# Kernel optimization log

Measured on AMD Instinct MI355X. Metric: run time of the kernel, lower is better.

The kernel has to match this reference:

```python
import jax, jax.numpy as jnp
import numpy as np

B, C_IN, H, W = 32, 64, 64, 64
D, O, S_SP, K = 256, 512, 4, 3


def setup_inputs() -> dict:
    key = jax.random.key(0)
    k1, k2, k3, k4, k5 = jax.random.split(key, 5)
    x = jax.random.normal(k1, (B, C_IN, H, W), dtype=jnp.float32)
    dictionary = jax.random.normal(k2, (D, C_IN, K, K), dtype=jnp.float32)
    lookup_coefficients = jax.random.normal(k3, (O, S_SP), dtype=jnp.float32)
    bias = jax.random.normal(k4, (O,), dtype=jnp.float32)
    lookup_indices = jax.random.randint(k5, (O, S_SP), 0, D)
    return {
        "x": x,
        "dictionary": dictionary,
        "lookup_coefficients": lookup_coefficients,
        "bias": bias,
        "lookup_indices": lookup_indices,
    }


def reference(x, dictionary, lookup_coefficients, bias, lookup_indices):
    # Dictionary conv: S has shape [B, D, H, W] (stride 1, padding 1, 3x3 kernel)
    S = jax.lax.conv_general_dilated(
        x, dictionary,
        window_strides=(1, 1),
        padding=((1, 1), (1, 1)),
        dimension_numbers=("NCHW", "OIHW", "NCHW"),
    )
    # Build dense [O, D] combine matrix via scatter-add (duplicate indices
    # accumulate, matching the original += loop), then one GEMM.
    rows = jnp.arange(O)[:, None]  # [O, 1] broadcast against [O, sparsity]
    Wc = jnp.zeros((O, D), dtype=S.dtype).at[rows, lookup_indices].add(lookup_coefficients)
    out = jnp.einsum("bdhw,od->bohw", S, Wc)
    return out + bias[None, :, None, None]
```

## Files before the change

### kernel.cpp

```cpp
#include <hip/hip_runtime.h>
#include <stdint.h>

#define NB 32
#define NC 64
#define NH 64
#define NW 64
#define NO 512
#define ND 256
#define HP 66

typedef __bf16 bf16x8 __attribute__((ext_vector_type(8)));
typedef short  s16x8  __attribute__((ext_vector_type(8)));
typedef float  f32x4  __attribute__((ext_vector_type(4)));
typedef uint32_t u32x2 __attribute__((ext_vector_type(2)));

__device__ __forceinline__ uint16_t f2bf(float f) {
  uint32_t u = __builtin_bit_cast(uint32_t, f);
  u += 0x7fffu + ((u >> 16) & 1u);
  return (uint16_t)(u >> 16);
}
__device__ __forceinline__ uint32_t pk2(float a, float b) {
  return (uint32_t)f2bf(a) | ((uint32_t)f2bf(b) << 16);
}
__device__ __forceinline__ float ubf_lo(uint32_t u) {
  return __builtin_bit_cast(float, u << 16);
}
__device__ __forceinline__ float ubf_hi(uint32_t u) {
  return __builtin_bit_cast(float, u & 0xffff0000u);
}

__device__ __forceinline__ void gld16(const uint16_t* g, uint16_t* l) {
  __builtin_amdgcn_global_load_lds(
      (const __attribute__((address_space(1))) void*)(g),
      (__attribute__((address_space(3))) void*)(l), 16, 0, 0);
}

__global__ void k_prep(const float* __restrict__ dict,
                       const float* __restrict__ x,
                       uint16_t*    __restrict__ Wd,
                       uint16_t*    __restrict__ xh) {
  const int bid = blockIdx.x;
  const int t = threadIdx.x;
  if (bid < ND) {
    const int d = bid;
#pragma unroll
    for (int j = 0; j < 3; ++j) {
      const int id = t + j * 256;
      if (id < 576) {
        const int c = id & 63, p = id >> 6;
        const int sl = ((p * ND + d) * 8 + ((c >> 3) ^ (d & 7))) * 8 + (c & 7);
        Wd[sl] = f2bf(dict[d * 576 + c * 9 + p]);
      }
    }
    return;
  }
  const int bh = bid - ND;
  const int b = bh / HP, hp = bh % HP;
  uint16_t* row = xh + (size_t)(b * HP + hp) * 4096;
  int4* r4 = reinterpret_cast<int4*>(row);
  if (hp == 0 || hp == HP - 1) {
    r4[t]       = int4{0, 0, 0, 0};
    r4[t + 256] = int4{0, 0, 0, 0};
    return;
  }
  __shared__ float tile[64][65];
  const int h = hp - 1;
  const int w = t & 63;
#pragma unroll
  for (int c = (t >> 6); c < 64; c += 4)
    tile[c][w] = x[((size_t)(b * NC + c) * NH + h) * NW + w];
  __syncthreads();
#pragma unroll
  for (int i = 0; i < 2; ++i) {
    const int s = t + i * 256;
    const int w2 = s >> 3, cb = s & 7;
    uint32_t dd[4];
#pragma unroll
    for (int j = 0; j < 4; ++j)
      dd[j] = pk2(tile[cb * 8 + 2 * j][w2], tile[cb * 8 + 2 * j + 1][w2]);
    r4[w2 * 8 + (cb ^ (w2 & 7))] =
        int4{(int)dd[0], (int)dd[1], (int)dd[2], (int)dd[3]};
  }
}

__global__ __launch_bounds__(512, 2) void k_conv(
    const uint16_t* __restrict__ xh,
    const uint16_t* __restrict__ Wd,
    const float*    __restrict__ coef,
    const int*      __restrict__ idx,
    const float*    __restrict__ bias,
    float*          __restrict__ out) {
  __shared__ __align__(16) uint16_t smem[74496];
  uint16_t* xs  = smem;
  uint16_t* asw = smem + 25344;
  uint8_t*  Sb  = (uint8_t*)smem;

  const int t = threadIdx.x;
  const int lane = t & 63;
  const int wid  = t >> 6;
  const int flat = blockIdx.x;
  const int s    = (flat & 7) * 64 + (flat >> 3);
  const int b    = s >> 4;
  const int hq   = s & 15;
  const int h0p  = hq * 4;

  if (t < 96) {
    const int r = t >> 4, sl = (t >> 3) & 1, j = t & 7;
    reinterpret_cast<int4*>(xs)[r * 528 + sl * 520 + j] = int4{0, 0, 0, 0};
  }
  {
#pragma unroll
    for (int j = 0; j < 6; ++j) {
      const int ch = wid * 6 + j;
      const int r = ch >> 3, k = ch & 7;
      gld16(xh + (size_t)(b * HP + h0p + r) * 4096 + k * 512 + lane * 8,
            xs + r * 4224 + 64 + k * 512);
    }
  }
  auto stage_a = [&](int g) {
#pragma unroll
    for (int j = 0; j < 12; ++j) {
      const int ch = wid * 12 + j;
      const int tap = ch >> 5, k = ch & 31;
      gld16(Wd + (size_t)(tap * 3 + g) * 16384 + k * 512 + lane * 8,
            asw + tap * 16384 + k * 512);
    }
  };
  stage_a(0);

  const int wd  = wid & 3;
  const int wn  = wid >> 2;
  const int l15 = lane & 15;
  const int lg  = lane >> 4;

  f32x4 acc[8][4];
#pragma unroll
  for (int pb = 0; pb < 8; ++pb)
#pragma unroll
    for (int db = 0; db < 4; ++db)
      acc[pb][db] = (f32x4){0.f, 0.f, 0.f, 0.f};

  __syncthreads();

#pragma unroll
  for (int g = 0; g < 3; ++g) {
    const int dw = g - 1;
#pragma unroll
    for (int q = 0; q < 2; ++q) {
      const int cbB = (q * 4 + lg) ^ ((l15 + dw) & 7);
      const uint16_t* xb = xs + (l15 + dw + 1) * 64 + cbB * 8;
      bf16x8 braw[4][4];
#pragma unroll
      for (int rr = 0; rr < 4; ++rr)
#pragma unroll
        for (int nw = 0; nw < 4; ++nw)
          braw[rr][nw] = __builtin_bit_cast(bf16x8,
              *reinterpret_cast<const s16x8*>(
                  xb + (wn * 2 + rr) * 4224 + nw * 1024));
      const int cbA = (q * 4 + lg) ^ (l15 & 7);
      const uint16_t* ab = asw + (wd * 64 + l15) * 64 + cbA * 8;
#pragma unroll
      for (int dh = 0; dh < 3; ++dh) {
        bf16x8 af[4];
#pragma unroll
        for (int db = 0; db < 4; ++db)
          af[db] = __builtin_bit_cast(bf16x8,
              *reinterpret_cast<const s16x8*>(
                  ab + dh * 16384 + db * 1024));
#pragma unroll
        for (int pb = 0; pb < 8; ++pb)
#pragma unroll
          for (int db = 0; db < 4; ++db)
            acc[pb][db] = __builtin_amdgcn_mfma_f32_16x16x32_bf16(
                braw[(pb >> 2) + dh][pb & 3], af[db], acc[pb][db], 0, 0, 0);
      }
    }
    if (g < 2) {
      __syncthreads();
      stage_a(g + 1);
      __syncthreads();
    }
  }

  __syncthreads();
#pragma unroll
  for (int pb = 0; pb < 8; ++pb) {
#pragma unroll
    for (int db = 0; db < 4; ++db) {
      const int d   = wd * 64 + db * 16 + l15;
      const int pix = (wn * 2 + (pb >> 2)) * 64 + (pb & 3) * 16 + lg * 4;
      u32x2 u;
      u[0] = pk2(acc[pb][db][0], acc[pb][db][1]);
      u[1] = pk2(acc[pb][db][2], acc[pb][db][3]);
      *reinterpret_cast<u32x2*>(
          Sb + d * 512 + ((pix * 2) ^ ((d & 7) << 4))) = u;
    }
  }
  __syncthreads();

  const int hrow = lane >> 4;
  const int wcol = (lane & 15) * 4;
#pragma unroll 4
  for (int oo = 0; oo < 64; ++oo) {
    const int o = wid * 64 + oo;
    const int4 iv = *reinterpret_cast<const int4*>(idx + o * 4);
    const f32x4 cv = *reinterpret_cast<const f32x4*>(coef + o * 4);
    const float bv = bias[o];
    f32x4 v = {bv, bv, bv, bv};
#define GATH(ROW, CS) do {                                                  \
      const int r_ = (ROW);                                                 \
      const u32x2 u_ = *reinterpret_cast<const u32x2*>(                     \
          Sb + r_ * 512 + ((lane * 8) ^ ((r_ & 7) << 4)));                  \
      const float c_ = (CS);                                                \
      v[0] += c_ * ubf_lo(u_[0]);  v[1] += c_ * ubf_hi(u_[0]);              \
      v[2] += c_ * ubf_lo(u_[1]);  v[3] += c_ * ubf_hi(u_[1]);              \
    } while (0)
    GATH(iv.x, cv[0]);
    GATH(iv.y, cv[1]);
    GATH(iv.z, cv[2]);
    GATH(iv.w, cv[3]);
#undef GATH
    float* dst = out + ((size_t)(b * NO + o) * NH + hq * 4 + hrow) * NW + wcol;
    __builtin_nontemporal_store(v, reinterpret_cast<f32x4*>(dst));
  }
}

extern "C" void kernel_launch(void* const* d_in, const int* in_sizes, int n_in,
                              void* d_out, int out_size, void* d_ws, size_t ws_size,
                              hipStream_t stream) {
  const float* x    = (const float*)d_in[0];
  const float* dict = (const float*)d_in[1];
  const float* coef = (const float*)d_in[2];
  const float* bias = (const float*)d_in[3];
  const int*   idx  = (const int*)d_in[4];
  float* out = (float*)d_out;

  uint16_t* xh = (uint16_t*)d_ws;
  uint16_t* Wd = (uint16_t*)((char*)d_ws + (18u << 20));

  hipLaunchKernelGGL(k_prep, dim3(ND + NB * HP), dim3(256), 0, stream,
                     dict, x, Wd, xh);
  hipLaunchKernelGGL(k_conv, dim3(512), dim3(512), 0, stream,
                     xh, Wd, coef, idx, bias, out);
}
```

Measured before the change: 99.67 us.

## Fuse input bf16 conversion and padding into conv kernel, drop xh workspace

The x-to-bf16 transpose and halo padding moves out of the prep kernel and into the conv kernel. Each block now loads its six fp32 input rows, transposes them through LDS scratch in the weight-tile region, and writes the swizzled bf16 layout directly. This removes the 18 MB intermediate write and read of xh and most of the prep launch. In exchange the conv kernel's prologue grows by extra barriers and serial LDS work, and each input row is read by several blocks in fp32, twice the bytes of bf16.

```diff
diff --git a/kernel.cpp b/kernel.cpp
--- a/kernel.cpp
+++ b/kernel.cpp
@@ -7,7 +7,6 @@
 #define NW 64
 #define NO 512
 #define ND 256
-#define HP 66
 
 typedef __bf16 bf16x8 __attribute__((ext_vector_type(8)));
 typedef short  s16x8  __attribute__((ext_vector_type(8)));
@@ -35,56 +34,23 @@
       (__attribute__((address_space(3))) void*)(l), 16, 0, 0);
 }
 
-__global__ void k_prep(const float* __restrict__ dict,
-                       const float* __restrict__ x,
-                       uint16_t*    __restrict__ Wd,
-                       uint16_t*    __restrict__ xh) {
-  const int bid = blockIdx.x;
+__global__ void k_prep_wd(const float* __restrict__ dict,
+                          uint16_t*    __restrict__ Wd) {
+  const int d = blockIdx.x;
   const int t = threadIdx.x;
-  if (bid < ND) {
-    const int d = bid;
-#pragma unroll
-    for (int j = 0; j < 3; ++j) {
-      const int id = t + j * 256;
-      if (id < 576) {
-        const int c = id & 63, p = id >> 6;
-        const int sl = ((p * ND + d) * 8 + ((c >> 3) ^ (d & 7))) * 8 + (c & 7);
-        Wd[sl] = f2bf(dict[d * 576 + c * 9 + p]);
-      }
-    }
-    return;
-  }
-  const int bh = bid - ND;
-  const int b = bh / HP, hp = bh % HP;
-  uint16_t* row = xh + (size_t)(b * HP + hp) * 4096;
-  int4* r4 = reinterpret_cast<int4*>(row);
-  if (hp == 0 || hp == HP - 1) {
-    r4[t]       = int4{0, 0, 0, 0};
-    r4[t + 256] = int4{0, 0, 0, 0};
-    return;
-  }
-  __shared__ float tile[64][65];
-  const int h = hp - 1;
-  const int w = t & 63;
-#pragma unroll
-  for (int c = (t >> 6); c < 64; c += 4)
-    tile[c][w] = x[((size_t)(b * NC + c) * NH + h) * NW + w];
-  __syncthreads();
-#pragma unroll
-  for (int i = 0; i < 2; ++i) {
-    const int s = t + i * 256;
-    const int w2 = s >> 3, cb = s & 7;
-    uint32_t dd[4];
-#pragma unroll
-    for (int j = 0; j < 4; ++j)
-      dd[j] = pk2(tile[cb * 8 + 2 * j][w2], tile[cb * 8 + 2 * j + 1][w2]);
-    r4[w2 * 8 + (cb ^ (w2 & 7))] =
-        int4{(int)dd[0], (int)dd[1], (int)dd[2], (int)dd[3]};
+#pragma unroll
+  for (int j = 0; j < 3; ++j) {
+    const int id = t + j * 256;
+    if (id < 576) {
+      const int c = id & 63, p = id >> 6;
+      const int sl = ((p * ND + d) * 8 + ((c >> 3) ^ (d & 7))) * 8 + (c & 7);
+      Wd[sl] = f2bf(dict[d * 576 + c * 9 + p]);
+    }
   }
 }
 
 __global__ __launch_bounds__(512, 2) void k_conv(
-    const uint16_t* __restrict__ xh,
+    const float*    __restrict__ x,
     const uint16_t* __restrict__ Wd,
     const float*    __restrict__ coef,
     const int*      __restrict__ idx,
@@ -108,15 +74,48 @@
     const int r = t >> 4, sl = (t >> 3) & 1, j = t & 7;
     reinterpret_cast<int4*>(xs)[r * 528 + sl * 520 + j] = int4{0, 0, 0, 0};
   }
+
   {
-#pragma unroll
-    for (int j = 0; j < 6; ++j) {
-      const int ch = wid * 6 + j;
-      const int r = ch >> 3, k = ch & 7;
-      gld16(xh + (size_t)(b * HP + h0p + r) * 4096 + k * 512 + lane * 8,
-            xs + r * 4224 + 64 + k * 512);
-    }
-  }
+    float* ft = reinterpret_cast<float*>(asw);
+    const f32x4 z4 = {0.f, 0.f, 0.f, 0.f};
+#pragma unroll
+    for (int rp = 0; rp < 3; ++rp) {
+#pragma unroll
+      for (int rr = 0; rr < 2; ++rr) {
+        const int r = rp * 2 + rr;
+        const int h = h0p + r - 1;
+        float* tile = ft + rr * 4160;
+        const int c = t >> 3, ws = (t & 7) * 8;
+        if ((unsigned)h < 64u) {
+          const float* src =
+              x + (((size_t)(b * NC + c)) * NH + h) * NW + ws;
+          *reinterpret_cast<f32x4*>(tile + c * 65 + ws) =
+              *reinterpret_cast<const f32x4*>(src);
+          *reinterpret_cast<f32x4*>(tile + c * 65 + ws + 4) =
+              *reinterpret_cast<const f32x4*>(src + 4);
+        } else {
+          *reinterpret_cast<f32x4*>(tile + c * 65 + ws) = z4;
+          *reinterpret_cast<f32x4*>(tile + c * 65 + ws + 4) = z4;
+        }
+      }
+      __syncthreads();
+#pragma unroll
+      for (int rr = 0; rr < 2; ++rr) {
+        const int r = rp * 2 + rr;
+        const float* tile = ft + rr * 4160;
+        const int w2 = t >> 3, cb = t & 7;
+        uint32_t dd[4];
+#pragma unroll
+        for (int j = 0; j < 4; ++j)
+          dd[j] = pk2(tile[(cb * 8 + 2 * j) * 65 + w2],
+                      tile[(cb * 8 + 2 * j + 1) * 65 + w2]);
+        reinterpret_cast<int4*>(xs)[r * 528 + 8 + w2 * 8 + (cb ^ (w2 & 7))] =
+            int4{(int)dd[0], (int)dd[1], (int)dd[2], (int)dd[3]};
+      }
+      __syncthreads();
+    }
+  }
+
   auto stage_a = [&](int g) {
 #pragma unroll
     for (int j = 0; j < 12; ++j) {
@@ -235,11 +234,9 @@
   const int*   idx  = (const int*)d_in[4];
   float* out = (float*)d_out;
 
-  uint16_t* xh = (uint16_t*)d_ws;
-  uint16_t* Wd = (uint16_t*)((char*)d_ws + (18u << 20));
-
-  hipLaunchKernelGGL(k_prep, dim3(ND + NB * HP), dim3(256), 0, stream,
-                     dict, x, Wd, xh);
+  uint16_t* Wd = (uint16_t*)d_ws;
+
+  hipLaunchKernelGGL(k_prep_wd, dim3(ND), dim3(256), 0, stream, dict, Wd);
   hipLaunchKernelGGL(k_conv, dim3(512), dim3(512), 0, stream,
-                     xh, Wd, coef, idx, bias, out);
-}
+                     x, Wd, coef, idx, bias, out);
+}
```

Measured after the change: 99.68 us. No clear change (+0.0%).
